# Performance work log

Hardware: AMD Instinct MI355X
Metric: run time of the kernel (lower is better)

## Reference

```python
import jax, jax.numpy as jnp
import numpy as np

E = 256  # embed_dim == input_chn (required by ln_ff broadcast)
B = 256
LAMBDA_INIT = float(0.8 - 0.6 * np.exp(-0.3 * 1.0))  # layer_index = 1


def rmsnorm(x, scale, d, eps=1e-8):
    # matches torch RMSNorm: rms = ||x||_2 / sqrt(d); x / (rms + eps) * scale
    norm = jnp.linalg.norm(x, axis=-1, keepdims=True)
    rms = norm * (d ** -0.5)
    return scale * (x / (rms + eps))


def setup_inputs() -> dict:
    key = jax.random.key(0)
    ks = jax.random.split(key, 12)
    x = jax.random.normal(ks[0], (B, E, E), jnp.float32)
    s = 0.02
    return {
        "x": x,
        "Wq": jax.random.normal(ks[1], (E, 2 * E), jnp.float32) * s,
        "bq": jnp.zeros((2 * E,), jnp.float32),
        "Wk": jax.random.normal(ks[2], (E, 2 * E), jnp.float32) * s,
        "bk": jnp.zeros((2 * E,), jnp.float32),
        "Wv": jax.random.normal(ks[3], (E, E), jnp.float32) * s,
        "bv": jnp.zeros((E,), jnp.float32),
        "lq1": jax.random.normal(ks[4], (E,), jnp.float32) * 0.1,
        "lk1": jax.random.normal(ks[5], (E,), jnp.float32) * 0.1,
        "lq2": jax.random.normal(ks[6], (E,), jnp.float32) * 0.1,
        "lk2": jax.random.normal(ks[7], (E,), jnp.float32) * 0.1,
        "ln_attn_scale": jnp.ones((E,), jnp.float32),
        "norm_scale": jnp.ones((E,), jnp.float32),
        "ln_ff_scale": jnp.ones((E,), jnp.float32),
        "W1": jax.random.normal(ks[8], (E, 4 * E), jnp.float32) * s,
        "b1": jnp.zeros((4 * E,), jnp.float32),
        "W2": jax.random.normal(ks[9], (4 * E, E), jnp.float32) * s,
        "b2": jnp.zeros((E,), jnp.float32),
    }


def reference(x, Wq, bq, Wk, bk, Wv, bv, lq1, lk1, lq2, lk2,
              ln_attn_scale, norm_scale, ln_ff_scale, W1, b1, W2, b2):
    scale = E ** -0.25
    # a = ln_attn(x^T)^T  (normalize over seq dim which equals E)
    a = jnp.swapaxes(rmsnorm(jnp.swapaxes(x, -1, -2), ln_attn_scale, E), -1, -2)
    # decompose: moving average kernel=5, stride=1, edge-replicate padding 2 on seq dim
    ap = jnp.pad(a, ((0, 0), (2, 2), (0, 0)), mode="edge")
    trend = (ap[:, 0:-4] + ap[:, 1:-3] + ap[:, 2:-2] + ap[:, 3:-1] + ap[:, 4:]) / 5.0
    seasonal = a - trend
    # Q from trend, K from seasonal, V from a; all projected along the seq(=E) dim
    q = jnp.swapaxes(trend, -1, -2) @ Wq + bq          # [B, C, 2E]
    q1, q2 = jnp.split(q, 2, axis=-1)
    k = jnp.swapaxes(seasonal, -1, -2) @ Wk + bk       # [B, C, 2E]
    k1, k2 = jnp.split(k, 2, axis=-1)
    v = jnp.swapaxes(a, -1, -2) @ Wv + bv              # [B, C, E]
    a1 = jnp.einsum("bce,bde->bcd", q1, k1) * scale    # [B, C, C]
    a2 = jnp.einsum("bce,bde->bcd", q2, k2) * scale
    lam = jnp.exp(jnp.sum(lq1 * lk1)) - jnp.exp(jnp.sum(lq2 * lk2)) + LAMBDA_INIT
    d = jax.nn.softmax(a1, axis=-1) - lam * jax.nn.softmax(a2, axis=-1)
    attn = rmsnorm(d @ v, norm_scale, E) * (1.0 - LAMBDA_INIT)  # [B, C, E]
    x = x + jnp.swapaxes(attn, -1, -2)
    # FFN branch: ln_ff over last dim (chn == E), then project along seq dim
    h = jnp.swapaxes(rmsnorm(x, ln_ff_scale, E), -1, -2)        # [B, C, E]
    h = jax.nn.silu(h @ W1 + b1) @ W2 + b2                      # [B, C, E]
    x = x + jnp.swapaxes(h, -1, -2)
    return x
```

## Files before the change

### kernel.cpp

```cpp
#include <hip/hip_runtime.h>
#include <math.h>

static constexpr int E = 256;
static constexpr int BTOT = 256;

typedef __bf16 bf16;
typedef __bf16 bf16x8 __attribute__((ext_vector_type(8)));
typedef __bf16 bf16x4 __attribute__((ext_vector_type(4)));
typedef float f32x4 __attribute__((ext_vector_type(4)));

__device__ __forceinline__ void gload16(const void* g, void* l) {
  __builtin_amdgcn_global_load_lds(
      (const __attribute__((address_space(1))) void*)g,
      (__attribute__((address_space(3))) void*)l, 16, 0, 0);
}

__device__ __forceinline__ void xcd_decode(int b, int NX, int nPanels, int& x, int& g) {
  if ((nPanels & 7) == 0) {
    int gLo = b & 7;
    int t2 = b >> 3;
    x = t2 % NX;
    g = (t2 / NX) * 8 + gLo;
  } else {
    x = b % NX;
    g = b / NX;
  }
}

__device__ __forceinline__ float fsig(float x) {
  return __fdividef(1.0f, 1.0f + __expf(-x));
}

__global__ __launch_bounds__(256) void k_wT(const float* __restrict__ src,
                                            bf16* __restrict__ dst, int R, int C) {
  __shared__ float lds[32][33];
  int tiles_c = C >> 5;
  int tc = blockIdx.x % tiles_c;
  int tr = blockIdx.x / tiles_c;
  int r0 = tr << 5, c0 = tc << 5;
  int t = threadIdx.x, cc = t & 31, rr0 = t >> 5;
#pragma unroll
  for (int p = 0; p < 4; ++p) {
    int rr = rr0 + p * 8;
    lds[rr][cc] = src[(size_t)(r0 + rr) * C + (c0 + cc)];
  }
  __syncthreads();
#pragma unroll
  for (int p = 0; p < 4; ++p) {
    int rr = rr0 + p * 8;
    dst[(size_t)(c0 + rr) * R + (r0 + cc)] = (bf16)lds[cc][rr];
  }
}

__global__ void k_lam(const float* lq1, const float* lk1, const float* lq2,
                      const float* lk2, float lambda_init, float* lamOut) {
  int t = threadIdx.x;
  float v1 = lq1[t] * lk1[t];
  float v2 = lq2[t] * lk2[t];
  __shared__ float s1[4], s2[4];
#pragma unroll
  for (int o = 32; o; o >>= 1) { v1 += __shfl_xor(v1, o); v2 += __shfl_xor(v2, o); }
  if ((t & 63) == 0) { s1[t >> 6] = v1; s2[t >> 6] = v2; }
  __syncthreads();
  if (t == 0) {
    float a = s1[0] + s1[1] + s1[2] + s1[3];
    float b = s2[0] + s2[1] + s2[2] + s2[3];
    *lamOut = expf(a) - expf(b) + lambda_init;
  }
}

__global__ __launch_bounds__(1024) void k_rmsA(const float* __restrict__ x, int batchBase,
                                               float* __restrict__ rinvA) {
  __shared__ float red[4][257];
  int lz = blockIdx.x;
  int g = batchBase + lz;
  int t = threadIdx.x, j = t & 255, qd = t >> 8;
  const float* xb = x + (size_t)g * E * E;
  float s = 0.f;
#pragma unroll 4
  for (int ii = 0; ii < 64; ++ii) {
    float v = xb[(size_t)(qd * 64 + ii) * E + j];
    s += v * v;
  }
  red[qd][j] = s;
  __syncthreads();
  if (qd == 0) {
    float tot = red[0][j] + red[1][j] + red[2][j] + red[3][j];
    rinvA[lz * E + j] = __fdividef(1.0f, sqrtf(tot) * 0.0625f + 1e-8f);
  }
}

__global__ __launch_bounds__(256) void k_prep(const float* __restrict__ x, int batchBase,
                                              const float* __restrict__ rinvA,
                                              const float* __restrict__ lnattn,
                                              bf16* __restrict__ a_t,
                                              bf16* __restrict__ tr_t, bf16* __restrict__ se_t) {
  __shared__ float lA[36][261];
  int lz = blockIdx.y, g = batchBase + lz;
  int i0 = blockIdx.x << 5;
  int t = threadIdx.x;
  const float* xb = x + (size_t)g * E * E;
  float rj = rinvA[lz * E + t];
#pragma unroll
  for (int rr = 0; rr < 36; ++rr) {
    int gi = i0 - 2 + rr;
    gi = gi < 0 ? 0 : (gi > 255 ? 255 : gi);
    float v = xb[(size_t)gi * E + t];
    lA[rr][t] = lnattn[gi] * v * rj;
  }
  __syncthreads();
  size_t bo = (size_t)lz * E * E;
  int ic = t & 31, jg = t >> 5;
#pragma unroll 4
  for (int jj = 0; jj < 32; ++jj) {
    int j = jg + jj * 8;
    float a0 = lA[ic][j], a1 = lA[ic + 1][j], a2 = lA[ic + 2][j];
    float a3 = lA[ic + 3][j], a4 = lA[ic + 4][j];
    float tr = (a0 + a1 + a2 + a3 + a4) * 0.2f;
    size_t o = bo + (size_t)j * E + i0 + ic;
    a_t[o] = (bf16)a2;
    tr_t[o] = (bf16)tr;
    se_t[o] = (bf16)(a2 - tr);
  }
}

__global__ __launch_bounds__(256) void gemm_qk(
    const bf16* __restrict__ A1, const bf16* __restrict__ A2,
    const bf16* __restrict__ B1, const bf16* __restrict__ B2,
    bf16* __restrict__ O1, bf16* __restrict__ O2,
    const float* __restrict__ bias1, const float* __restrict__ bias2, int cnt) {
  __shared__ __align__(128) bf16 As[128][64];
  __shared__ __align__(128) bf16 Bs[128][64];
  int xdec, gdec;
  xcd_decode(blockIdx.x, 4, 4 * cnt, xdec, gdec);
  int lz = gdec >> 2;
  int sel = (gdec >> 1) & 1;
  int mb = (gdec & 1) << 7, nb = xdec << 7;
  const bf16* Ab = (sel ? A2 : A1) + (size_t)lz * 65536;
  const bf16* Bb = sel ? B2 : B1;
  bf16* Out = (sel ? O2 : O1) + (size_t)lz * 131072;
  const float* biasN = sel ? bias2 : bias1;
  int t = threadIdx.x, lane = t & 63, wv = t >> 6;
  int wr = wv >> 1, wc = wv & 1;
  int lrow = lane >> 3;
  int kel = ((lane & 7) ^ lrow) << 3;
  f32x4 acc[4][4];
  const f32x4 z4 = {0.f, 0.f, 0.f, 0.f};
#pragma unroll
  for (int a = 0; a < 4; ++a)
#pragma unroll
    for (int b = 0; b < 4; ++b) acc[a][b] = z4;
  for (int k0 = 0; k0 < 256; k0 += 64) {
    __syncthreads();
#pragma unroll
    for (int i = 0; i < 4; ++i) {
      int rb = i * 32 + wv * 8;
      gload16(&Ab[(size_t)(mb + rb + lrow) * 256 + k0 + kel], &As[rb][0]);
      gload16(&Bb[(size_t)(nb + rb + lrow) * 256 + k0 + kel], &Bs[rb][0]);
    }
    __syncthreads();
    __builtin_amdgcn_s_setprio(1);
#pragma unroll
    for (int kk = 0; kk < 2; ++kk) {
      int kb = (kk * 64 + ((lane >> 4) << 4)) ^ ((lane & 7) << 4);
      bf16x8 af[4], bfr[4];
#pragma unroll
      for (int mi = 0; mi < 4; ++mi)
        af[mi] = *(const bf16x8*)((const char*)As + (wr * 64 + mi * 16 + (lane & 15)) * 128 + kb);
#pragma unroll
      for (int ni = 0; ni < 4; ++ni)
        bfr[ni] = *(const bf16x8*)((const char*)Bs + (wc * 64 + ni * 16 + (lane & 15)) * 128 + kb);
#pragma unroll
      for (int mi = 0; mi < 4; ++mi)
#pragma unroll
        for (int ni = 0; ni < 4; ++ni)
          acc[mi][ni] = __builtin_amdgcn_mfma_f32_16x16x32_bf16(af[mi], bfr[ni],
                                                                acc[mi][ni], 0, 0, 0);
    }
    __builtin_amdgcn_s_setprio(0);
  }
  int colB = nb + wc * 64 + (lane & 15);
  int rowB = mb + wr * 64 + ((lane >> 4) << 2);
#pragma unroll
  for (int mi = 0; mi < 4; ++mi) {
#pragma unroll
    for (int ni = 0; ni < 4; ++ni) {
      int col = colB + ni * 16;
      float bN = biasN[col];
#pragma unroll
      for (int r = 0; r < 4; ++r) {
        int row = rowB + mi * 16 + r;
        Out[(size_t)row * 512 + col] = (bf16)(acc[mi][ni][r] + bN);
      }
    }
  }
}

template <int EPI>
__global__ __launch_bounds__(256) void gemm_bt(
    const bf16* __restrict__ A, int lda, size_t aStride,
    const bf16* __restrict__ B, int ldb, size_t bStride,
    bf16* __restrict__ Out, int ldo, size_t oStride, int K,
    const float* __restrict__ biasN, const float* __restrict__ biasM,
    int NX, int NY, int nPanels) {
  __shared__ __align__(128) bf16 As[128][64];
  __shared__ __align__(128) bf16 Bs[128][64];
  int xdec, gdec;
  xcd_decode(blockIdx.x, NX, nPanels, xdec, gdec);
  int lz = gdec / NY;
  int mb = (gdec % NY) << 7, nb = xdec << 7;
  const bf16* Ab = A + (size_t)lz * aStride;
  const bf16* Bb = B + (size_t)lz * bStride;
  int t = threadIdx.x, lane = t & 63, wv = t >> 6;
  int wr = wv >> 1, wc = wv & 1;
  int lrow = lane >> 3;
  int kel = ((lane & 7) ^ lrow) << 3;
  f32x4 acc[4][4];
  const f32x4 z4 = {0.f, 0.f, 0.f, 0.f};
#pragma unroll
  for (int a = 0; a < 4; ++a)
#pragma unroll
    for (int b = 0; b < 4; ++b) acc[a][b] = z4;
  for (int k0 = 0; k0 < K; k0 += 64) {
    __syncthreads();
#pragma unroll
    for (int i = 0; i < 4; ++i) {
      int rb = i * 32 + wv * 8;
      gload16(&Ab[(size_t)(mb + rb + lrow) * lda + k0 + kel], &As[rb][0]);
      gload16(&Bb[(size_t)(nb + rb + lrow) * ldb + k0 + kel], &Bs[rb][0]);
    }
    __syncthreads();
    __builtin_amdgcn_s_setprio(1);
#pragma unroll
    for (int kk = 0; kk < 2; ++kk) {
      int kb = (kk * 64 + ((lane >> 4) << 4)) ^ ((lane & 7) << 4);
      bf16x8 af[4], bfr[4];
#pragma unroll
      for (int mi = 0; mi < 4; ++mi)
        af[mi] = *(const bf16x8*)((const char*)As + (wr * 64 + mi * 16 + (lane & 15)) * 128 + kb);
#pragma unroll
      for (int ni = 0; ni < 4; ++ni)
        bfr[ni] = *(const bf16x8*)((const char*)Bs + (wc * 64 + ni * 16 + (lane & 15)) * 128 + kb);
#pragma unroll
      for (int mi = 0; mi < 4; ++mi)
#pragma unroll
        for (int ni = 0; ni < 4; ++ni)
          acc[mi][ni] = __builtin_amdgcn_mfma_f32_16x16x32_bf16(af[mi], bfr[ni],
                                                                acc[mi][ni], 0, 0, 0);
    }
    __builtin_amdgcn_s_setprio(0);
  }
  int colB = nb + wc * 64 + (lane & 15);
  int rowB = mb + wr * 64 + ((lane >> 4) << 2);
#pragma unroll
  for (int mi = 0; mi < 4; ++mi) {
#pragma unroll
    for (int ni = 0; ni < 4; ++ni) {
      int col = colB + ni * 16;
      float bN = 0.f;
      if constexpr (EPI == 1) bN = biasN[col];
#pragma unroll
      for (int r = 0; r < 4; ++r) {
        int row = rowB + mi * 16 + r;
        float v = acc[mi][ni][r];
        if constexpr (EPI == 1) {
          Out[(size_t)lz * oStride + (size_t)row * ldo + col] = (bf16)(v + bN);
        } else {
          Out[(size_t)lz * oStride + (size_t)row * ldo + col] = (bf16)(v + biasM[row]);
        }
      }
    }
  }
}

__global__ __launch_bounds__(512) void k_attn(const bf16* __restrict__ q,
                                              const bf16* __restrict__ km,
                                              const bf16* __restrict__ vT,
                                              const float* __restrict__ x, int batchBase,
                                              const float* __restrict__ nscale,
                                              const float* __restrict__ lamPtr, float oml,
                                              bf16* __restrict__ Y, int nPanels) {
  __shared__ __align__(128) bf16 As[128][64];
  __shared__ __align__(128) bf16 Bs[256][64];
  __shared__ float red[4][128];
  __shared__ __align__(128) char Pb[65536];
  int xdec, lz;
  xcd_decode(blockIdx.x, 2, nPanels, xdec, lz);
  int mb = xdec << 7;
  const bf16* qb = q + (size_t)lz * E * 512;
  const bf16* kb = km + (size_t)lz * E * 512;
  int t = threadIdx.x, lane = t & 63, wv = t >> 6;
  int wr = wv >> 2, wc = wv & 3;
  int lrow = lane >> 3;
  int kel = ((lane & 7) ^ lrow) << 3;
  int l15 = lane & 15, l4 = lane >> 4;
  f32x4 acc1[4][4], acc2[4][4];
  const f32x4 z4 = {0.f, 0.f, 0.f, 0.f};
#pragma unroll
  for (int a = 0; a < 4; ++a)
#pragma unroll
    for (int b = 0; b < 4; ++b) { acc1[a][b] = z4; acc2[a][b] = z4; }
#pragma unroll
  for (int mat = 0; mat < 2; ++mat) {
    f32x4(*acc)[4] = mat == 0 ? acc1 : acc2;
    const bf16* qm = qb + mat * 256;
    const bf16* kmm = kb + mat * 256;
    for (int k0 = 0; k0 < 256; k0 += 64) {
      __syncthreads();
#pragma unroll
      for (int i = 0; i < 2; ++i) {
        int rb = i * 64 + wv * 8;
        gload16(&qm[(size_t)(mb + rb + lrow) * 512 + k0 + kel], &As[rb][0]);
      }
#pragma unroll
      for (int i = 0; i < 4; ++i) {
        int rb = i * 64 + wv * 8;
        gload16(&kmm[(size_t)(rb + lrow) * 512 + k0 + kel], &Bs[rb][0]);
      }
      __syncthreads();
      __builtin_amdgcn_s_setprio(1);
#pragma unroll
      for (int kk = 0; kk < 2; ++kk) {
        int kb2 = (kk * 64 + (l4 << 4)) ^ ((lane & 7) << 4);
        bf16x8 af[4], bfr[4];
#pragma unroll
        for (int mi = 0; mi < 4; ++mi)
          af[mi] = *(const bf16x8*)((const char*)As + (wr * 64 + mi * 16 + l15) * 128 + kb2);
#pragma unroll
        for (int ni = 0; ni < 4; ++ni)
          bfr[ni] = *(const bf16x8*)((const char*)Bs + (wc * 64 + ni * 16 + l15) * 128 + kb2);
#pragma unroll
        for (int mi = 0; mi < 4; ++mi)
#pragma unroll
          for (int ni = 0; ni < 4; ++ni)
            acc[mi][ni] = __builtin_amdgcn_mfma_f32_16x16x32_bf16(af[mi], bfr[ni],
                                                                  acc[mi][ni], 0, 0, 0);
      }
      __builtin_amdgcn_s_setprio(0);
    }
  }
  float lam = *lamPtr;
  int rbase = wr * 64 + (l4 << 2);
  float inv1[4][4], inv2[4][4];
  __syncthreads();
#pragma unroll
  for (int mat = 0; mat < 2; ++mat) {
    f32x4(*acc)[4] = mat == 0 ? acc1 : acc2;
    float(*inv)[4] = mat == 0 ? inv1 : inv2;
    float tmp[4][4];
#pragma unroll
    for (int mi = 0; mi < 4; ++mi)
#pragma unroll
      for (int r = 0; r < 4; ++r) {
        float m = fmaxf(fmaxf(acc[mi][0][r], acc[mi][1][r]),
                        fmaxf(acc[mi][2][r], acc[mi][3][r]));
        m = fmaxf(m, __shfl_xor(m, 1));
        m = fmaxf(m, __shfl_xor(m, 2));
        m = fmaxf(m, __shfl_xor(m, 4));
        m = fmaxf(m, __shfl_xor(m, 8));
        tmp[mi][r] = m;
      }
    if (l15 == 0) {
#pragma unroll
      for (int mi = 0; mi < 4; ++mi)
#pragma unroll
        for (int r = 0; r < 4; ++r) red[wc][rbase + mi * 16 + r] = tmp[mi][r];
    }
    __syncthreads();
#pragma unroll
    for (int mi = 0; mi < 4; ++mi)
#pragma unroll
      for (int r = 0; r < 4; ++r) {
        int rw = rbase + mi * 16 + r;
        tmp[mi][r] = fmaxf(fmaxf(red[0][rw], red[1][rw]), fmaxf(red[2][rw], red[3][rw]));
      }
    __syncthreads();
#pragma unroll
    for (int mi = 0; mi < 4; ++mi)
#pragma unroll
      for (int r = 0; r < 4; ++r) {
        float m = tmp[mi][r], s = 0.f;
#pragma unroll
        for (int ni = 0; ni < 4; ++ni) {
          float p = __expf(0.25f * (acc[mi][ni][r] - m));
          acc[mi][ni][r] = p;
          s += p;
        }
        s += __shfl_xor(s, 1);
        s += __shfl_xor(s, 2);
        s += __shfl_xor(s, 4);
        s += __shfl_xor(s, 8);
        tmp[mi][r] = s;
      }
    if (l15 == 0) {
#pragma unroll
      for (int mi = 0; mi < 4; ++mi)
#pragma unroll
        for (int r = 0; r < 4; ++r) red[wc][rbase + mi * 16 + r] = tmp[mi][r];
    }
    __syncthreads();
#pragma unroll
    for (int mi = 0; mi < 4; ++mi)
#pragma unroll
      for (int r = 0; r < 4; ++r) {
        int rw = rbase + mi * 16 + r;
        inv[mi][r] = __fdividef(1.0f, red[0][rw] + red[1][rw] + red[2][rw] + red[3][rw]);
      }
    __syncthreads();
  }
#pragma unroll
  for (int mi = 0; mi < 4; ++mi)
#pragma unroll
    for (int ni = 0; ni < 4; ++ni) {
      int d = wc * 64 + ni * 16 + l15;
#pragma unroll
      for (int r = 0; r < 4; ++r) {
        int c = rbase + mi * 16 + r;
        bf16 p = (bf16)(acc1[mi][ni][r] * inv1[mi][r] - lam * acc2[mi][ni][r] * inv2[mi][r]);
        *(bf16*)(Pb + c * 512 + ((2 * d) ^ ((c & 7) << 4))) = p;
      }
    }
  asm volatile("s_waitcnt lgkmcnt(0)" ::: "memory");
  const bf16* Bb = vT + (size_t)lz * E * E;
  f32x4 acc[4][4];
#pragma unroll
  for (int a = 0; a < 4; ++a)
#pragma unroll
    for (int b = 0; b < 4; ++b) acc[a][b] = z4;
  for (int k0 = 0; k0 < 256; k0 += 64) {
    __syncthreads();
#pragma unroll
    for (int i = 0; i < 4; ++i) {
      int rb = i * 64 + wv * 8;
      gload16(&Bb[(size_t)(rb + lrow) * E + k0 + kel], &Bs[rb][0]);
    }
    __syncthreads();
    __builtin_amdgcn_s_setprio(1);
#pragma unroll
    for (int kk = 0; kk < 2; ++kk) {
      int kb2 = (kk * 64 + (l4 << 4)) ^ ((lane & 7) << 4);
      bf16x8 af[4], bfr[4];
#pragma unroll
      for (int mi = 0; mi < 4; ++mi) {
        int c = wr * 64 + mi * 16 + l15;
        int kbP = (k0 * 2 + kk * 64 + (l4 << 4)) ^ ((c & 7) << 4);
        af[mi] = *(const bf16x8*)(Pb + c * 512 + kbP);
      }
#pragma unroll
      for (int ni = 0; ni < 4; ++ni)
        bfr[ni] = *(const bf16x8*)((const char*)Bs + (wc * 64 + ni * 16 + l15) * 128 + kb2);
#pragma unroll
      for (int mi = 0; mi < 4; ++mi)
#pragma unroll
        for (int ni = 0; ni < 4; ++ni)
          acc[mi][ni] = __builtin_amdgcn_mfma_f32_16x16x32_bf16(af[mi], bfr[ni],
                                                                acc[mi][ni], 0, 0, 0);
    }
    __builtin_amdgcn_s_setprio(0);
  }
  float rowinv[4][4];
#pragma unroll
  for (int mi = 0; mi < 4; ++mi)
#pragma unroll
    for (int r = 0; r < 4; ++r) {
      float s = 0.f;
#pragma unroll
      for (int ni = 0; ni < 4; ++ni) {
        float v = acc[mi][ni][r];
        s += v * v;
      }
      s += __shfl_xor(s, 1);
      s += __shfl_xor(s, 2);
      s += __shfl_xor(s, 4);
      s += __shfl_xor(s, 8);
      rowinv[mi][r] = s;
    }
  __syncthreads();
  if (l15 == 0) {
#pragma unroll
    for (int mi = 0; mi < 4; ++mi)
#pragma unroll
      for (int r = 0; r < 4; ++r) red[wc][rbase + mi * 16 + r] = rowinv[mi][r];
  }
  __syncthreads();
#pragma unroll
  for (int mi = 0; mi < 4; ++mi)
#pragma unroll
    for (int r = 0; r < 4; ++r) {
      int rw = rbase + mi * 16 + r;
      float tot = red[0][rw] + red[1][rw] + red[2][rw] + red[3][rw];
      rowinv[mi][r] = oml * __fdividef(1.0f, sqrtf(tot) * 0.0625f + 1e-8f);
    }
  size_t bo = (size_t)lz * E * E;
  const float* xb = x + (size_t)(batchBase + lz) * E * E;
#pragma unroll
  for (int mi = 0; mi < 4; ++mi)
#pragma unroll
    for (int ni = 0; ni < 4; ++ni) {
      int col = wc * 64 + ni * 16 + l15;
      float ns = nscale[col];
      int row0 = mb + rbase + mi * 16;
      f32x4 xv = *(const f32x4*)&xb[(size_t)col * E + row0];
#pragma unroll
      for (int r = 0; r < 4; ++r) {
        size_t o = bo + (size_t)(row0 + r) * E + col;
        Y[o] = (bf16)(xv[r] + ns * acc[mi][ni][r] * rowinv[mi][r]);
      }
    }
}

__global__ __launch_bounds__(256) void k_ffnorm(const bf16* __restrict__ Y,
                                                const float* __restrict__ lnff,
                                                bf16* __restrict__ xn) {
  __shared__ float red[8][33];
  __shared__ float rl[32];
  int lz = blockIdx.y;
  int i0 = blockIdx.x << 5;
  int t = threadIdx.x, ic = t & 31, jg = t >> 5;
  size_t bo = (size_t)lz * E * E;
  float s = 0.f;
#pragma unroll 4
  for (int jj = 0; jj < 32; ++jj) {
    int j = jg + jj * 8;
    float v = (float)Y[bo + (size_t)j * E + i0 + ic];
    s += v * v;
  }
  red[jg][ic] = s;
  __syncthreads();
  if (jg == 0) {
    float tot = 0.f;
#pragma unroll
    for (int g2 = 0; g2 < 8; ++g2) tot += red[g2][ic];
    rl[ic] = __fdividef(1.0f, sqrtf(tot) * 0.0625f + 1e-8f);
  }
  __syncthreads();
  float rinv = rl[ic];
#pragma unroll 4
  for (int jj = 0; jj < 32; ++jj) {
    int j = jg + jj * 8;
    size_t o = bo + (size_t)j * E + i0 + ic;
    xn[o] = (bf16)(lnff[j] * (float)Y[o] * rinv);
  }
}

__global__ __launch_bounds__(1024) void k_ffn(const bf16* __restrict__ xn,
                                              const bf16* __restrict__ W1T,
                                              const bf16* __restrict__ W2T,
                                              const float* __restrict__ b1,
                                              const float* __restrict__ b2,
                                              const bf16* __restrict__ Y,
                                              int batchBase, float* __restrict__ out) {
  __shared__ __align__(128) char arena[131072];
  char* Hb = arena;
  char* xnL = arena + 32768;
  char* S0 = arena + 65536;
  char* S1 = arena + 98304;
  int bid = blockIdx.x;
  int lz = bid >> 2;
  int c0 = (bid & 3) << 6;
  const bf16* xb = xn + (size_t)lz * E * E + (size_t)c0 * E;
  int t = threadIdx.x, lane = t & 63, wv = t >> 6;
  int lrow = lane >> 3;
  int kel = ((lane & 7) ^ lrow) << 3;
  int l15 = lane & 15, l4 = lane >> 4, l7 = lane & 7;
  int wr1 = wv >> 3, wc1 = wv & 7;
  int wr2 = wv >> 1, wc2 = wv & 1;

  float b1v[4][2];
#pragma unroll
  for (int ch = 0; ch < 4; ++ch)
#pragma unroll
    for (int ni = 0; ni < 2; ++ni)
      b1v[ch][ni] = b1[ch * 256 + wc1 * 32 + ni * 16 + l15];

#pragma unroll
  for (int j = 0; j < 2; ++j) {
    int lin = wv * 2 + j;
    int ksub = lin >> 3, rg = (lin & 7) * 8;
    gload16(&xb[(size_t)(rg + lrow) * E + ksub * 64 + kel], xnL + ksub * 8192 + rg * 128);
  }
#pragma unroll
  for (int i = 0; i < 2; ++i) {
    int rb = i * 128 + wv * 8;
    gload16(&W1T[(size_t)(rb + lrow) * 256 + kel], S0 + rb * 128);
  }

  f32x4 acc2[2][2];
  const f32x4 z4 = {0.f, 0.f, 0.f, 0.f};
  acc2[0][0] = z4; acc2[0][1] = z4; acc2[1][0] = z4; acc2[1][1] = z4;
  int cur = 0;

  for (int ch = 0; ch < 4; ++ch) {
    f32x4 acc1[2][2];
    acc1[0][0] = z4; acc1[0][1] = z4; acc1[1][0] = z4; acc1[1][1] = z4;
    for (int k = 0; k < 4; ++k) {
      char* Sn = cur ? S0 : S1;
      if (k < 3) {
#pragma unroll
        for (int i = 0; i < 2; ++i) {
          int rb = i * 128 + wv * 8;
          gload16(&W1T[(size_t)(ch * 256 + rb + lrow) * 256 + (k + 1) * 64 + kel], Sn + rb * 128);
        }
      } else {
#pragma unroll
        for (int i = 0; i < 2; ++i) {
          int rb = i * 128 + wv * 8;
          gload16(&W2T[(size_t)(rb + lrow) * 1024 + ch * 256 + kel], Sn + rb * 128);
        }
      }
      asm volatile("s_waitcnt vmcnt(2)" ::: "memory");
      __builtin_amdgcn_s_barrier();
      char* Sc = cur ? S1 : S0;
#pragma unroll
      for (int kk = 0; kk < 2; ++kk) {
        int kb = (kk * 64 + (l4 << 4)) ^ (l7 << 4);
        bf16x8 af[2], bfr[2];
#pragma unroll
        for (int mi = 0; mi < 2; ++mi)
          af[mi] = *(const bf16x8*)(xnL + k * 8192 + (wr1 * 32 + mi * 16 + l15) * 128 + kb);
#pragma unroll
        for (int ni = 0; ni < 2; ++ni)
          bfr[ni] = *(const bf16x8*)(Sc + (wc1 * 32 + ni * 16 + l15) * 128 + kb);
#pragma unroll
        for (int mi = 0; mi < 2; ++mi)
#pragma unroll
          for (int ni = 0; ni < 2; ++ni)
            acc1[mi][ni] = __builtin_amdgcn_mfma_f32_16x16x32_bf16(af[mi], bfr[ni],
                                                                   acc1[mi][ni], 0, 0, 0);
      }
      __builtin_amdgcn_s_barrier();
      cur ^= 1;
    }
#pragma unroll
    for (int mi = 0; mi < 2; ++mi)
#pragma unroll
      for (int ni = 0; ni < 2; ++ni) {
        int e1 = wc1 * 32 + ni * 16 + l15;
        float bN = b1v[ch][ni];
#pragma unroll
        for (int r = 0; r < 4; ++r) {
          int c = wr1 * 32 + mi * 16 + l4 * 4 + r;
          float u = acc1[mi][ni][r] + bN;
          float h = u * fsig(u);
          int bo2 = c * 512 + ((((e1 >> 3) ^ (c & 7)) << 4) | ((e1 & 7) * 2));
          *(bf16*)(Hb + bo2) = (bf16)h;
        }
      }
    asm volatile("s_waitcnt lgkmcnt(0)" ::: "memory");
    for (int k = 0; k < 4; ++k) {
      char* Sn = cur ? S0 : S1;
      bool isLast = (ch == 3) && (k == 3);
      if (k < 3) {
#pragma unroll
        for (int i = 0; i < 2; ++i) {
          int rb = i * 128 + wv * 8;
          gload16(&W2T[(size_t)(rb + lrow) * 1024 + ch * 256 + (k + 1) * 64 + kel], Sn + rb * 128);
        }
      } else if (ch < 3) {
#pragma unroll
        for (int i = 0; i < 2; ++i) {
          int rb = i * 128 + wv * 8;
          gload16(&W1T[(size_t)((ch + 1) * 256 + rb + lrow) * 256 + kel], Sn + rb * 128);
        }
      }
      if (isLast) asm volatile("s_waitcnt vmcnt(0)" ::: "memory");
      else        asm volatile("s_waitcnt vmcnt(2)" ::: "memory");
      __builtin_amdgcn_s_barrier();
      char* Sc = cur ? S1 : S0;
#pragma unroll
      for (int kk = 0; kk < 2; ++kk) {
        int kb = (kk * 64 + (l4 << 4)) ^ (l7 << 4);
        int kbH = (k * 128 + kk * 64 + (l4 << 4)) ^ (l7 << 4);
        bf16x8 af[2], bfr[2];
#pragma unroll
        for (int mi = 0; mi < 2; ++mi)
          af[mi] = *(const bf16x8*)(Sc + (wr2 * 32 + mi * 16 + l15) * 128 + kb);
#pragma unroll
        for (int ni = 0; ni < 2; ++ni)
          bfr[ni] = *(const bf16x8*)(Hb + (wc2 * 32 + ni * 16 + l15) * 512 + kbH);
#pragma unroll
        for (int mi = 0; mi < 2; ++mi)
#pragma unroll
          for (int ni = 0; ni < 2; ++ni)
            acc2[mi][ni] = __builtin_amdgcn_mfma_f32_16x16x32_bf16(af[mi], bfr[ni],
                                                                   acc2[mi][ni], 0, 0, 0);
      }
      __builtin_amdgcn_s_barrier();
      cur ^= 1;
    }
  }
  const bf16* Yb = Y + (size_t)lz * E * E;
  float* ob = out + (size_t)(batchBase + lz) * E * E;
#pragma unroll
  for (int mi = 0; mi < 2; ++mi) {
    int e2b = wr2 * 32 + mi * 16 + l4 * 4;
    f32x4 bv = *(const f32x4*)&b2[e2b];
#pragma unroll
    for (int ni = 0; ni < 2; ++ni) {
      int c = c0 + wc2 * 32 + ni * 16 + l15;
      bf16x4 yv = *(const bf16x4*)&Yb[(size_t)c * E + e2b];
#pragma unroll
      for (int r = 0; r < 4; ++r)
        ob[(size_t)(e2b + r) * E + c] = acc2[mi][ni][r] + bv[r] + (float)yv[r];
    }
  }
}

extern "C" void kernel_launch(void* const* d_in, const int* in_sizes, int n_in,
                              void* d_out, int out_size, void* d_ws, size_t ws_size,
                              hipStream_t stream) {
  const float* x = (const float*)d_in[0];
  const float* Wq = (const float*)d_in[1];
  const float* bq = (const float*)d_in[2];
  const float* Wk = (const float*)d_in[3];
  const float* bk = (const float*)d_in[4];
  const float* Wv = (const float*)d_in[5];
  const float* bv = (const float*)d_in[6];
  const float* lq1 = (const float*)d_in[7];
  const float* lk1 = (const float*)d_in[8];
  const float* lq2 = (const float*)d_in[9];
  const float* lk2 = (const float*)d_in[10];
  const float* lnattn = (const float*)d_in[11];
  const float* nscale = (const float*)d_in[12];
  const float* lnff = (const float*)d_in[13];
  const float* W1 = (const float*)d_in[14];
  const float* b1 = (const float*)d_in[15];
  const float* W2 = (const float*)d_in[16];
  const float* b2 = (const float*)d_in[17];
  float* out = (float*)d_out;

  char* ws = (char*)d_ws;
  size_t off = 0;
  auto alloc = [&](size_t bytes) {
    size_t o = off;
    off += (bytes + 255) & ~(size_t)255;
    return o;
  };
  size_t oWqT = alloc(512 * 256 * 2);
  size_t oWkT = alloc(512 * 256 * 2);
  size_t oWvT = alloc(256 * 256 * 2);
  size_t oW1T = alloc(1024 * 256 * 2);
  size_t oW2T = alloc(256 * 1024 * 2);
  size_t oLam = alloc(256);
  size_t weightEnd = off;

  const size_t szH = (size_t)E * E * 2;
  const size_t szQ = (size_t)E * 512 * 2;
  const size_t szRi = 1024;
  size_t perBatch = 4 * szH + 2 * szQ + szRi;
  size_t avail = ws_size > weightEnd ? ws_size - weightEnd : 0;
  int NB = (int)(avail / perBatch);
  if (NB > BTOT) NB = BTOT;
  if (NB < 1) NB = 1;

  size_t o = weightEnd;
  auto allocN = [&](size_t bytes) {
    size_t r = o;
    o += bytes * (size_t)NB;
    return r;
  };
  bf16* pA = (bf16*)(ws + allocN(szH));
  bf16* pTr = (bf16*)(ws + allocN(szH));
  bf16* pSe = (bf16*)(ws + allocN(szH));
  bf16* pVT = (bf16*)(ws + allocN(szH));
  size_t oQK = allocN(2 * szQ);
  float* pRiA = (float*)(ws + allocN(szRi));

  bf16* pQ = (bf16*)(ws + oQK);
  bf16* pK = (bf16*)(ws + oQK + (size_t)NB * szQ);
  bf16* pY = pA;
  bf16* pXn = pSe;

  bf16* pWqT = (bf16*)(ws + oWqT);
  bf16* pWkT = (bf16*)(ws + oWkT);
  bf16* pWvT = (bf16*)(ws + oWvT);
  bf16* pW1T = (bf16*)(ws + oW1T);
  bf16* pW2T = (bf16*)(ws + oW2T);
  float* pLam = (float*)(ws + oLam);

  const float LAMBDA_INIT = 0.8f - 0.6f * expf(-0.3f);
  const float OML = 1.0f - LAMBDA_INIT;

  k_wT<<<dim3((256 / 32) * (512 / 32)), 256, 0, stream>>>(Wq, pWqT, 256, 512);
  k_wT<<<dim3((256 / 32) * (512 / 32)), 256, 0, stream>>>(Wk, pWkT, 256, 512);
  k_wT<<<dim3((256 / 32) * (256 / 32)), 256, 0, stream>>>(Wv, pWvT, 256, 256);
  k_wT<<<dim3((256 / 32) * (1024 / 32)), 256, 0, stream>>>(W1, pW1T, 256, 1024);
  k_wT<<<dim3((1024 / 32) * (256 / 32)), 256, 0, stream>>>(W2, pW2T, 1024, 256);
  k_lam<<<1, 256, 0, stream>>>(lq1, lk1, lq2, lk2, LAMBDA_INIT, pLam);

  for (int base = 0; base < BTOT; base += NB) {
    int cnt = BTOT - base < NB ? BTOT - base : NB;
    k_rmsA<<<dim3(cnt), 1024, 0, stream>>>(x, base, pRiA);
    k_prep<<<dim3(8, cnt), 256, 0, stream>>>(x, base, pRiA, lnattn, pA, pTr, pSe);
    gemm_qk<<<dim3(16 * cnt), 256, 0, stream>>>(pTr, pSe, pWqT, pWkT, pQ, pK, bq, bk, cnt);
    gemm_bt<2><<<dim3(2 * 2 * cnt), 256, 0, stream>>>(pWvT, 256, 0, pA, 256, 65536,
        pVT, 256, 65536, 256, nullptr, bv, 2, 2, 2 * cnt);
    k_attn<<<dim3(2 * cnt), 512, 0, stream>>>(pQ, pK, pVT, x, base, nscale, pLam,
                                              OML, pY, cnt);
    k_ffnorm<<<dim3(8, cnt), 256, 0, stream>>>(pY, lnff, pXn);
    k_ffn<<<dim3(4 * cnt), 1024, 0, stream>>>(pXn, pW1T, pW2T, b1, b2, pY, base, out);
  }
}
```

Baseline: 485.4 us.

## Shrink attention kernel LDS by staging P in halves and aliasing buffers

```diff
diff --git a/kernel.cpp b/kernel.cpp
--- a/kernel.cpp
+++ b/kernel.cpp
@@ -273,17 +273,18 @@
   }
 }
 
-__global__ __launch_bounds__(512) void k_attn(const bf16* __restrict__ q,
-                                              const bf16* __restrict__ km,
-                                              const bf16* __restrict__ vT,
-                                              const float* __restrict__ x, int batchBase,
-                                              const float* __restrict__ nscale,
-                                              const float* __restrict__ lamPtr, float oml,
-                                              bf16* __restrict__ Y, int nPanels) {
-  __shared__ __align__(128) bf16 As[128][64];
-  __shared__ __align__(128) bf16 Bs[256][64];
-  __shared__ float red[4][128];
-  __shared__ __align__(128) char Pb[65536];
+__global__ __launch_bounds__(512, 4) void k_attn(const bf16* __restrict__ q,
+                                                 const bf16* __restrict__ km,
+                                                 const bf16* __restrict__ vT,
+                                                 const float* __restrict__ x, int batchBase,
+                                                 const float* __restrict__ nscale,
+                                                 const float* __restrict__ lamPtr, float oml,
+                                                 bf16* __restrict__ Y, int nPanels) {
+  __shared__ __align__(128) char arena[67584];
+  char* BsB = arena;
+  char* AsB = arena + 32768;
+  char* Ph  = arena + 32768;
+  float* red = (float*)(arena + 65536);
   int xdec, lz;
   xcd_decode(blockIdx.x, 2, nPanels, xdec, lz);
   int mb = xdec << 7;
@@ -310,12 +311,12 @@
 #pragma unroll
       for (int i = 0; i < 2; ++i) {
         int rb = i * 64 + wv * 8;
-        gload16(&qm[(size_t)(mb + rb + lrow) * 512 + k0 + kel], &As[rb][0]);
+        gload16(&qm[(size_t)(mb + rb + lrow) * 512 + k0 + kel], AsB + rb * 128);
       }
 #pragma unroll
       for (int i = 0; i < 4; ++i) {
         int rb = i * 64 + wv * 8;
-        gload16(&kmm[(size_t)(rb + lrow) * 512 + k0 + kel], &Bs[rb][0]);
+        gload16(&kmm[(size_t)(rb + lrow) * 512 + k0 + kel], BsB + rb * 128);
       }
       __syncthreads();
       __builtin_amdgcn_s_setprio(1);
@@ -325,10 +326,10 @@
         bf16x8 af[4], bfr[4];
 #pragma unroll
         for (int mi = 0; mi < 4; ++mi)
-          af[mi] = *(const bf16x8*)((const char*)As + (wr * 64 + mi * 16 + l15) * 128 + kb2);
+          af[mi] = *(const bf16x8*)(AsB + (wr * 64 + mi * 16 + l15) * 128 + kb2);
 #pragma unroll
         for (int ni = 0; ni < 4; ++ni)
-          bfr[ni] = *(const bf16x8*)((const char*)Bs + (wc * 64 + ni * 16 + l15) * 128 + kb2);
+          bfr[ni] = *(const bf16x8*)(BsB + (wc * 64 + ni * 16 + l15) * 128 + kb2);
 #pragma unroll
         for (int mi = 0; mi < 4; ++mi)
 #pragma unroll
@@ -364,7 +365,7 @@
 #pragma unroll
       for (int mi = 0; mi < 4; ++mi)
 #pragma unroll
-        for (int r = 0; r < 4; ++r) red[wc][rbase + mi * 16 + r] = tmp[mi][r];
+        for (int r = 0; r < 4; ++r) red[wc * 128 + rbase + mi * 16 + r] = tmp[mi][r];
     }
     __syncthreads();
 #pragma unroll
@@ -372,7 +373,8 @@
 #pragma unroll
       for (int r = 0; r < 4; ++r) {
         int rw = rbase + mi * 16 + r;
-        tmp[mi][r] = fmaxf(fmaxf(red[0][rw], red[1][rw]), fmaxf(red[2][rw], red[3][rw]));
+        tmp[mi][r] = fmaxf(fmaxf(red[rw], red[128 + rw]),
+                           fmaxf(red[256 + rw], red[384 + rw]));
       }
     __syncthreads();
 #pragma unroll
@@ -396,7 +398,7 @@
 #pragma unroll
       for (int mi = 0; mi < 4; ++mi)
 #pragma unroll
-        for (int r = 0; r < 4; ++r) red[wc][rbase + mi * 16 + r] = tmp[mi][r];
+        for (int r = 0; r < 4; ++r) red[wc * 128 + rbase + mi * 16 + r] = tmp[mi][r];
     }
     __syncthreads();
 #pragma unroll
@@ -404,59 +406,75 @@
 #pragma unroll
       for (int r = 0; r < 4; ++r) {
         int rw = rbase + mi * 16 + r;
-        inv[mi][r] = __fdividef(1.0f, red[0][rw] + red[1][rw] + red[2][rw] + red[3][rw]);
+        inv[mi][r] = __fdividef(1.0f, red[rw] + red[128 + rw] + red[256 + rw] + red[384 + rw]);
       }
     __syncthreads();
   }
+  bf16x4 pP[4][4];
 #pragma unroll
   for (int mi = 0; mi < 4; ++mi)
 #pragma unroll
-    for (int ni = 0; ni < 4; ++ni) {
-      int d = wc * 64 + ni * 16 + l15;
-#pragma unroll
-      for (int r = 0; r < 4; ++r) {
-        int c = rbase + mi * 16 + r;
-        bf16 p = (bf16)(acc1[mi][ni][r] * inv1[mi][r] - lam * acc2[mi][ni][r] * inv2[mi][r]);
-        *(bf16*)(Pb + c * 512 + ((2 * d) ^ ((c & 7) << 4))) = p;
-      }
-    }
-  asm volatile("s_waitcnt lgkmcnt(0)" ::: "memory");
+    for (int ni = 0; ni < 4; ++ni)
+#pragma unroll
+      for (int r = 0; r < 4; ++r)
+        pP[mi][ni][r] = (bf16)(acc1[mi][ni][r] * inv1[mi][r] -
+                               lam * acc2[mi][ni][r] * inv2[mi][r]);
   const bf16* Bb = vT + (size_t)lz * E * E;
   f32x4 acc[4][4];
 #pragma unroll
   for (int a = 0; a < 4; ++a)
 #pragma unroll
     for (int b = 0; b < 4; ++b) acc[a][b] = z4;
-  for (int k0 = 0; k0 < 256; k0 += 64) {
+#pragma unroll
+  for (int half = 0; half < 2; ++half) {
+    if ((wc >> 1) == half) {
+      int dBase = (wc & 1) << 6;
+#pragma unroll
+      for (int mi = 0; mi < 4; ++mi)
+#pragma unroll
+        for (int ni = 0; ni < 4; ++ni) {
+          int dRel = dBase + ni * 16 + l15;
+#pragma unroll
+          for (int r = 0; r < 4; ++r) {
+            int c = rbase + mi * 16 + r;
+            *(bf16*)(Ph + c * 256 + ((2 * dRel) ^ ((c & 7) << 4))) = pP[mi][ni][r];
+          }
+        }
+    }
+    asm volatile("s_waitcnt lgkmcnt(0)" ::: "memory");
+#pragma unroll
+    for (int k0h = 0; k0h < 128; k0h += 64) {
+      __syncthreads();
+#pragma unroll
+      for (int i = 0; i < 4; ++i) {
+        int rb = i * 64 + wv * 8;
+        gload16(&Bb[(size_t)(rb + lrow) * E + half * 128 + k0h + kel], BsB + rb * 128);
+      }
+      __syncthreads();
+      __builtin_amdgcn_s_setprio(1);
+#pragma unroll
+      for (int kk = 0; kk < 2; ++kk) {
+        int kb2 = (kk * 64 + (l4 << 4)) ^ ((lane & 7) << 4);
+        bf16x8 af[4], bfr[4];
+#pragma unroll
+        for (int mi = 0; mi < 4; ++mi) {
+          int c = wr * 64 + mi * 16 + l15;
+          int kbP = (k0h * 2 + kk * 64 + (l4 << 4)) ^ ((c & 7) << 4);
+          af[mi] = *(const bf16x8*)(Ph + c * 256 + kbP);
+        }
+#pragma unroll
+        for (int ni = 0; ni < 4; ++ni)
+          bfr[ni] = *(const bf16x8*)(BsB + (wc * 64 + ni * 16 + l15) * 128 + kb2);
+#pragma unroll
+        for (int mi = 0; mi < 4; ++mi)
+#pragma unroll
+          for (int ni = 0; ni < 4; ++ni)
+            acc[mi][ni] = __builtin_amdgcn_mfma_f32_16x16x32_bf16(af[mi], bfr[ni],
+                                                                  acc[mi][ni], 0, 0, 0);
+      }
+      __builtin_amdgcn_s_setprio(0);
+    }
     __syncthreads();
-#pragma unroll
-    for (int i = 0; i < 4; ++i) {
-      int rb = i * 64 + wv * 8;
-      gload16(&Bb[(size_t)(rb + lrow) * E + k0 + kel], &Bs[rb][0]);
-    }
-    __syncthreads();
-    __builtin_amdgcn_s_setprio(1);
-#pragma unroll
-    for (int kk = 0; kk < 2; ++kk) {
-      int kb2 = (kk * 64 + (l4 << 4)) ^ ((lane & 7) << 4);
-      bf16x8 af[4], bfr[4];
-#pragma unroll
-      for (int mi = 0; mi < 4; ++mi) {
-        int c = wr * 64 + mi * 16 + l15;
-        int kbP = (k0 * 2 + kk * 64 + (l4 << 4)) ^ ((c & 7) << 4);
-        af[mi] = *(const bf16x8*)(Pb + c * 512 + kbP);
-      }
-#pragma unroll
-      for (int ni = 0; ni < 4; ++ni)
-        bfr[ni] = *(const bf16x8*)((const char*)Bs + (wc * 64 + ni * 16 + l15) * 128 + kb2);
-#pragma unroll
-      for (int mi = 0; mi < 4; ++mi)
-#pragma unroll
-        for (int ni = 0; ni < 4; ++ni)
-          acc[mi][ni] = __builtin_amdgcn_mfma_f32_16x16x32_bf16(af[mi], bfr[ni],
-                                                                acc[mi][ni], 0, 0, 0);
-    }
-    __builtin_amdgcn_s_setprio(0);
   }
   float rowinv[4][4];
 #pragma unroll
@@ -475,12 +493,11 @@
       s += __shfl_xor(s, 8);
       rowinv[mi][r] = s;
     }
-  __syncthreads();
   if (l15 == 0) {
 #pragma unroll
     for (int mi = 0; mi < 4; ++mi)
 #pragma unroll
-      for (int r = 0; r < 4; ++r) red[wc][rbase + mi * 16 + r] = rowinv[mi][r];
+      for (int r = 0; r < 4; ++r) red[wc * 128 + rbase + mi * 16 + r] = rowinv[mi][r];
   }
   __syncthreads();
 #pragma unroll
@@ -488,7 +505,7 @@
 #pragma unroll
     for (int r = 0; r < 4; ++r) {
       int rw = rbase + mi * 16 + r;
-      float tot = red[0][rw] + red[1][rw] + red[2][rw] + red[3][rw];
+      float tot = red[rw] + red[128 + rw] + red[256 + rw] + red[384 + rw];
       rowinv[mi][r] = oml * __fdividef(1.0f, sqrtf(tot) * 0.0625f + 1e-8f);
     }
   size_t bo = (size_t)lz * E * E;
```

New measurement: 676.3 us. 39.3% more time.
